# Kernel tuning notes

Measured on AMD Instinct MI355X. Metric: run time of the kernel, lower is better.

## Reference

```python
import jax, jax.numpy as jnp
import numpy as np

N_NODES = 50000
N_EDGES = 400000
FEAT = 64      # irreps_in modeled as 64 scalar channels; head_dim == FEAT
HEADS = 4


def setup_inputs() -> dict:
    key = jax.random.key(0)
    k = jax.random.split(key, 7)
    x = jax.random.normal(k[0], (N_NODES, FEAT), dtype=jnp.float32)
    edge_index = jax.random.randint(k[1], (2, N_EDGES), 0, N_NODES, dtype=jnp.int32)
    s = 1.0 / np.sqrt(FEAT)
    Wq = jax.random.normal(k[2], (HEADS, FEAT, FEAT), dtype=jnp.float32) * s
    Wk = jax.random.normal(k[3], (HEADS, FEAT, FEAT), dtype=jnp.float32) * s
    Wv = jax.random.normal(k[4], (HEADS, FEAT, FEAT), dtype=jnp.float32) * s
    Wout = jax.random.normal(k[5], (FEAT, FEAT), dtype=jnp.float32) * s
    return {"x": x, "Wq": Wq, "Wk": Wk, "Wv": Wv, "Wout": Wout, "edge_index": edge_index}


def reference(x, Wq, Wk, Wv, Wout, edge_index):
    # Per-node attention over graph neighbors. The torch module pads neighbors
    # into degree buckets and runs SDPA per bucket; mathematically this is a
    # segment (per-receiver) softmax over incoming edges, which we compute
    # directly without padding or bucket loops.
    sender, receiver = edge_index[0], edge_index[1]
    n = x.shape[0]
    scale = x.shape[1] ** -0.5  # head_dim == FEAT in the original module

    Q = jnp.einsum('nf,hfd->hnd', x, Wq)  # (H, N, F)
    K = jnp.einsum('nf,hfd->hnd', x, Wk)
    V = jnp.einsum('nf,hfd->hnd', x, Wv)

    # Edge scores: q_receiver . k_sender per head -> (E, H)
    s = jnp.einsum('hef,hef->eh', Q[:, receiver], K[:, sender]) * scale

    # Numerically stable segment softmax over each receiver's neighborhood.
    m = jax.ops.segment_max(s, receiver, num_segments=n)          # (N, H)
    p = jnp.exp(s - m[receiver])                                   # (E, H)
    denom = jax.ops.segment_sum(p, receiver, num_segments=n)      # (N, H)
    alpha = p / denom[receiver]                                    # (E, H)

    # Weighted message aggregation: (H, E, F) scattered to (H, N, F).
    msg = alpha.T[:, :, None] * V[:, sender]
    agg = jax.vmap(lambda mh: jax.ops.segment_sum(mh, receiver, num_segments=n))(msg)

    out = jnp.nan_to_num(agg.mean(axis=0))  # deg-0 nodes contribute zeros
    return x + out @ Wout
```

## Files before the change

kernel.cpp:

```cpp
#include <hip/hip_runtime.h>

#define FEAT 64
#define HEADS 4
#define CAP 64
#define LROW 520
#define TSTR 80

typedef __attribute__((ext_vector_type(8))) short short8;
typedef __attribute__((ext_vector_type(8))) __bf16 bf16x8;
typedef __attribute__((ext_vector_type(4))) float floatx4;
typedef __attribute__((ext_vector_type(2))) float float2v;
typedef unsigned short ushortT;

static __device__ __forceinline__ unsigned short f2bf(float f) {
    union { float f; unsigned int u; } v; v.f = f;
    unsigned int u = v.u;
    u = u + 0x7fffu + ((u >> 16) & 1u);
    return (unsigned short)(u >> 16);
}
static __device__ __forceinline__ float bfl(unsigned int u) {
    union { unsigned int u; float f; } v; v.u = u << 16; return v.f;
}
static __device__ __forceinline__ float bfh(unsigned int u) {
    union { unsigned int u; float f; } v; v.u = u & 0xffff0000u; return v.f;
}

__global__ __launch_bounds__(256) void k_init(const float* __restrict__ Wq,
        const float* __restrict__ Wk, const float* __restrict__ Wv,
        const float* __restrict__ Wout, short8* __restrict__ Wpack,
        short8* __restrict__ WoutPack, int4* __restrict__ deg4, int nslots) {
    int t = blockIdx.x * 256 + threadIdx.x;
    if (t < nslots) deg4[t] = make_int4(0, 0, 0, 0);
    int o = t;
    if (o < 12 * 2 * 4 * 64) {
        int lane = o & 63, dt = (o >> 6) & 3, kb = (o >> 8) & 1, m = o >> 9;
        int mat = m >> 2, h = m & 3;
        const float* src = (mat == 0) ? Wq : (mat == 1) ? Wk : Wv;
        src += (size_t)h * 64 * 64;
        int d = dt * 16 + (lane & 15);
        int kbase = kb * 32 + (lane >> 4) * 8;
        short8 val;
#pragma unroll
        for (int j = 0; j < 8; j++)
            val[j] = (short)f2bf(src[(kbase + j) * 64 + d]);
        Wpack[o] = val;
    } else if (o < 6144 + 512) {
        int idx = o - 6144;
        int lane = idx & 63, kb = (idx >> 6) & 1, nt = idx >> 7;
        int d = nt * 16 + (lane & 15);
        int kbase = kb * 32 + (lane >> 4) * 8;
        short8 val;
#pragma unroll
        for (int j = 0; j < 8; j++)
            val[j] = (short)f2bf(Wout[(kbase + j) * 64 + d]);
        WoutPack[idx] = val;
    }
}

__global__ __launch_bounds__(256) void k_qkv(const float* __restrict__ x,
        const short8* __restrict__ Wpack, const int* __restrict__ send,
        const int* __restrict__ recv, int* __restrict__ deg,
        int* __restrict__ srt, ushortT* __restrict__ Qb, ushortT* __restrict__ KVb,
        int E) {
    __shared__ ushortT lds[16 * LROW];
    int e = blockIdx.x * 256 + threadIdx.x;
    if (e < E) {
        int r = recv[e];
        int pos = atomicAdd(&deg[r], 1);
        if (pos < CAP) srt[(size_t)r * CAP + pos] = send[e];
    }

    int w = threadIdx.x >> 6, lane = threadIdx.x & 63;
    int quad = lane >> 4, lrow = lane & 15;
    int ntile = blockIdx.x * 16;
    const float* xrow = x + (size_t)(ntile + lrow) * 64 + quad * 8;
    float4 fa = *(const float4*)(xrow);
    float4 fb = *(const float4*)(xrow + 4);
    float4 fc = *(const float4*)(xrow + 32);
    float4 fd = *(const float4*)(xrow + 36);
    short8 a0 = {(short)f2bf(fa.x), (short)f2bf(fa.y), (short)f2bf(fa.z), (short)f2bf(fa.w),
                 (short)f2bf(fb.x), (short)f2bf(fb.y), (short)f2bf(fb.z), (short)f2bf(fb.w)};
    short8 a1 = {(short)f2bf(fc.x), (short)f2bf(fc.y), (short)f2bf(fc.z), (short)f2bf(fc.w),
                 (short)f2bf(fd.x), (short)f2bf(fd.y), (short)f2bf(fd.z), (short)f2bf(fd.w)};
    bf16x8 X0 = __builtin_bit_cast(bf16x8, a0);
    bf16x8 X1 = __builtin_bit_cast(bf16x8, a1);
#pragma unroll
    for (int mat = 0; mat < 3; mat++) {
        int m = mat * 4 + w;
#pragma unroll
        for (int dt = 0; dt < 4; dt++) {
            floatx4 acc = {0.f, 0.f, 0.f, 0.f};
            short8 b0 = Wpack[((m * 2 + 0) * 4 + dt) * 64 + lane];
            short8 b1 = Wpack[((m * 2 + 1) * 4 + dt) * 64 + lane];
            acc = __builtin_amdgcn_mfma_f32_16x16x32_bf16(
                __builtin_bit_cast(bf16x8, b0), X0, acc, 0, 0, 0);
            acc = __builtin_amdgcn_mfma_f32_16x16x32_bf16(
                __builtin_bit_cast(bf16x8, b1), X1, acc, 0, 0, 0);
            if (mat == 0) {
                unsigned int u01 = (unsigned)f2bf(acc[0] * 0.125f)
                                 | ((unsigned)f2bf(acc[1] * 0.125f) << 16);
                unsigned int u23 = (unsigned)f2bf(acc[2] * 0.125f)
                                 | ((unsigned)f2bf(acc[3] * 0.125f) << 16);
                *(uint2*)&lds[lrow * LROW + w * 64 + dt * 16 + quad * 4]
                    = make_uint2(u01, u23);
            } else {
                int p = __builtin_amdgcn_cvt_pk_fp8_f32(acc[0], acc[1], 0, false);
                p = __builtin_amdgcn_cvt_pk_fp8_f32(acc[2], acc[3], p, true);
                int slot = w * 16 + dt * 4 + quad;
                *(unsigned int*)&lds[lrow * LROW + 256 + slot * 4 + ((mat == 2) ? 2 : 0)]
                    = (unsigned int)p;
            }
        }
    }
    __syncthreads();
    {
        int u = threadIdx.x;
#pragma unroll
        for (int rep = 0; rep < 2; rep++, u += 256) {
            int row = u >> 5, idx = u & 31;
            uint4 val = *(const uint4*)&lds[row * LROW + idx * 8];
            *(uint4*)(Qb + ((size_t)(ntile + row)) * 256 + idx * 8) = val;
        }
    }
    {
        uint4* KVq = (uint4*)KVb;
        int u = threadIdx.x;
#pragma unroll
        for (int rep = 0; rep < 2; rep++, u += 256) {
            int row = u >> 5, idx = u & 31;
            uint4 val = *(const uint4*)&lds[row * LROW + 256 + idx * 8];
            KVq[(size_t)(ntile + row) * 32 + idx] = val;
        }
    }
}

__global__ __launch_bounds__(256) void k_attn(const ushortT* __restrict__ Qb,
        const ushortT* __restrict__ KVb, const short8* __restrict__ WoutPack,
        const int* __restrict__ deg, const int* __restrict__ srt,
        const float* __restrict__ x, float* __restrict__ out, int N) {
    __shared__ ushortT tl[16 * TSTR];
    int w = threadIdx.x >> 6, lane = threadIdx.x & 63;
    int rb = blockIdx.x * 16;
    const uint2* KV2 = (const uint2*)KVb;

    for (int rr = 0; rr < 4; rr++) {
        int ridx = w * 4 + rr;
        int r = rb + ridx;
        uint2 qu = ((const uint2*)(Qb + (size_t)r * 256))[lane];
        float q0 = bfl(qu.x), q1 = bfh(qu.x);
        float q2 = bfl(qu.y), q3 = bfh(qu.y);
        float a0 = 0.f, a1 = 0.f, a2 = 0.f, a3 = 0.f, den = 0.f;
        const int* myslots = srt + (size_t)r * CAP;
        int d = min(deg[r], CAP);

#define PROC(kv)                                                          \
    {                                                                     \
        float2v kA = __builtin_amdgcn_cvt_pk_f32_fp8(kv.x, false);        \
        float2v kB = __builtin_amdgcn_cvt_pk_f32_fp8(kv.x, true);         \
        float2v vA = __builtin_amdgcn_cvt_pk_f32_fp8(kv.y, false);        \
        float2v vB = __builtin_amdgcn_cvt_pk_f32_fp8(kv.y, true);         \
        float sp = q0 * kA.x + q1 * kA.y + q2 * kB.x + q3 * kB.y;         \
        sp += __shfl_xor(sp, 1);                                          \
        sp += __shfl_xor(sp, 2);                                          \
        sp += __shfl_xor(sp, 4);                                          \
        sp += __shfl_xor(sp, 8);                                          \
        float p = __expf(sp);                                             \
        den += p;                                                         \
        a0 += p * vA.x; a1 += p * vA.y;                                   \
        a2 += p * vB.x; a3 += p * vB.y;                                   \
    }
        int i = 0;
        for (; i + 3 < d; i += 4) {
            int4 s4 = *(const int4*)(myslots + i);
            uint2 kv0 = KV2[(size_t)s4.x * 64 + lane];
            uint2 kv1 = KV2[(size_t)s4.y * 64 + lane];
            uint2 kv2 = KV2[(size_t)s4.z * 64 + lane];
            uint2 kv3 = KV2[(size_t)s4.w * 64 + lane];
            PROC(kv0) PROC(kv1) PROC(kv2) PROC(kv3)
        }
        for (; i < d; i++) {
            uint2 kv = KV2[(size_t)myslots[i] * 64 + lane];
            PROC(kv)
        }
#undef PROC
        float inv = (den > 0.f) ? 0.25f / den : 0.f;
        a0 *= inv; a1 *= inv; a2 *= inv; a3 *= inv;
        a0 += __shfl_xor(a0, 16); a1 += __shfl_xor(a1, 16);
        a2 += __shfl_xor(a2, 16); a3 += __shfl_xor(a3, 16);
        a0 += __shfl_xor(a0, 32); a1 += __shfl_xor(a1, 32);
        a2 += __shfl_xor(a2, 32); a3 += __shfl_xor(a3, 32);
        if (lane < 16) {
            unsigned int u01 = (unsigned)f2bf(a0) | ((unsigned)f2bf(a1) << 16);
            unsigned int u23 = (unsigned)f2bf(a2) | ((unsigned)f2bf(a3) << 16);
            *(uint2*)&tl[ridx * TSTR + lane * 4] = make_uint2(u01, u23);
        }
    }
    __syncthreads();

    int q = lane >> 4, c = lane & 15;
    short8 ta0 = *(const short8*)&tl[c * TSTR + q * 8];
    short8 ta1 = *(const short8*)&tl[c * TSTR + 32 + q * 8];
    short8 tb0 = WoutPack[(w * 2 + 0) * 64 + lane];
    short8 tb1 = WoutPack[(w * 2 + 1) * 64 + lane];
    floatx4 acc = {0.f, 0.f, 0.f, 0.f};
    acc = __builtin_amdgcn_mfma_f32_16x16x32_bf16(
        __builtin_bit_cast(bf16x8, ta0), __builtin_bit_cast(bf16x8, tb0), acc, 0, 0, 0);
    acc = __builtin_amdgcn_mfma_f32_16x16x32_bf16(
        __builtin_bit_cast(bf16x8, ta1), __builtin_bit_cast(bf16x8, tb1), acc, 0, 0, 0);
#pragma unroll
    for (int reg = 0; reg < 4; reg++) {
        size_t idx = (size_t)(rb + q * 4 + reg) * 64 + w * 16 + c;
        out[idx] = x[idx] + acc[reg];
    }
}

extern "C" void kernel_launch(void* const* d_in, const int* in_sizes, int n_in,
                              void* d_out, int out_size, void* d_ws, size_t ws_size,
                              hipStream_t stream) {
    const float* x    = (const float*)d_in[0];
    const float* Wq   = (const float*)d_in[1];
    const float* Wk   = (const float*)d_in[2];
    const float* Wv   = (const float*)d_in[3];
    const float* Wout = (const float*)d_in[4];
    const int*   ei   = (const int*)d_in[5];
    int N = in_sizes[0] / FEAT;
    int E = in_sizes[5] / 2;
    const int* send = ei;
    const int* recv = ei + E;

    char* ws = (char*)d_ws;
    size_t o = 0;
    auto alloc = [&](size_t bytes) {
        void* p = ws + o;
        o = (o + bytes + 255) & ~(size_t)255;
        return p;
    };
    ushortT* Qb      = (ushortT*)alloc((size_t)N * 256 * 2);
    ushortT* KVb     = (ushortT*)alloc((size_t)N * 512);
    short8* Wpack    = (short8*)alloc(6144 * sizeof(short8));
    short8* WoutPack = (short8*)alloc(512 * sizeof(short8));
    int* deg         = (int*)alloc((size_t)((N + 3) & ~3) * 4);
    int* srt         = (int*)alloc((size_t)N * CAP * 4);

    int nslots = ((N + 3) & ~3) / 4;
    k_init<<<64, 256, 0, stream>>>(Wq, Wk, Wv, Wout, Wpack, WoutPack,
                                   (int4*)deg, nslots);
    k_qkv<<<N / 16, 256, 0, stream>>>(x, Wpack, send, recv, deg, srt, Qb, KVb, E);
    k_attn<<<N / 16, 256, 0, stream>>>(Qb, KVb, WoutPack, deg, srt, x,
                                       (float*)d_out, N);
}
```

Measured before the change: 157.3 us.

## Process two edges per wavefront with 16-byte KV loads in attention kernel

Each wavefront now splits into two half-waves that each handle a different neighbor edge. Every lane loads a uint4 with 8 K and 8 V fp8 values instead of a uint2 with 4 of each. This halves the per-edge shuffle-reduction depth and the number of loop iterations, and uses wider loads. In exchange it adds extra cross-half shuffles at the end, masked tail handling, and higher register use for the 8 accumulators.

```diff
diff --git a/kernel.cpp b/kernel.cpp
--- a/kernel.cpp
+++ b/kernel.cpp
@@ -140,59 +140,81 @@
         const float* __restrict__ x, float* __restrict__ out, int N) {
     __shared__ ushortT tl[16 * TSTR];
     int w = threadIdx.x >> 6, lane = threadIdx.x & 63;
+    int el = lane & 31, e_sel = lane >> 5, jj = lane & 7;
     int rb = blockIdx.x * 16;
-    const uint2* KV2 = (const uint2*)KVb;
+    const uint4* KV4 = (const uint4*)KVb;
 
     for (int rr = 0; rr < 4; rr++) {
         int ridx = w * 4 + rr;
         int r = rb + ridx;
-        uint2 qu = ((const uint2*)(Qb + (size_t)r * 256))[lane];
-        float q0 = bfl(qu.x), q1 = bfh(qu.x);
-        float q2 = bfl(qu.y), q3 = bfh(qu.y);
-        float a0 = 0.f, a1 = 0.f, a2 = 0.f, a3 = 0.f, den = 0.f;
+        uint4 qu = ((const uint4*)(Qb + (size_t)r * 256))[el];
+        float q0 = bfl(qu.x), q1 = bfh(qu.x), q2 = bfl(qu.y), q3 = bfh(qu.y);
+        float q4 = bfl(qu.z), q5 = bfh(qu.z), q6 = bfl(qu.w), q7 = bfh(qu.w);
+        float a0 = 0.f, a1 = 0.f, a2 = 0.f, a3 = 0.f;
+        float a4 = 0.f, a5 = 0.f, a6 = 0.f, a7 = 0.f, den = 0.f;
         const int* myslots = srt + (size_t)r * CAP;
         int d = min(deg[r], CAP);
 
-#define PROC(kv)                                                          \
+#define PROC2(kv, pmask)                                                  \
     {                                                                     \
         float2v kA = __builtin_amdgcn_cvt_pk_f32_fp8(kv.x, false);        \
         float2v kB = __builtin_amdgcn_cvt_pk_f32_fp8(kv.x, true);         \
-        float2v vA = __builtin_amdgcn_cvt_pk_f32_fp8(kv.y, false);        \
-        float2v vB = __builtin_amdgcn_cvt_pk_f32_fp8(kv.y, true);         \
-        float sp = q0 * kA.x + q1 * kA.y + q2 * kB.x + q3 * kB.y;         \
+        float2v kC = __builtin_amdgcn_cvt_pk_f32_fp8(kv.z, false);        \
+        float2v kD = __builtin_amdgcn_cvt_pk_f32_fp8(kv.z, true);         \
+        float sp = q0 * kA.x + q1 * kA.y + q2 * kB.x + q3 * kB.y          \
+                 + q4 * kC.x + q5 * kC.y + q6 * kD.x + q7 * kD.y;         \
         sp += __shfl_xor(sp, 1);                                          \
         sp += __shfl_xor(sp, 2);                                          \
         sp += __shfl_xor(sp, 4);                                          \
-        sp += __shfl_xor(sp, 8);                                          \
         float p = __expf(sp);                                             \
+        p = (pmask) ? p : 0.f;                                            \
+        float2v vA = __builtin_amdgcn_cvt_pk_f32_fp8(kv.y, false);        \
+        float2v vB = __builtin_amdgcn_cvt_pk_f32_fp8(kv.y, true);         \
+        float2v vC = __builtin_amdgcn_cvt_pk_f32_fp8(kv.w, false);        \
+        float2v vD = __builtin_amdgcn_cvt_pk_f32_fp8(kv.w, true);         \
         den += p;                                                         \
-        a0 += p * vA.x; a1 += p * vA.y;                                   \
-        a2 += p * vB.x; a3 += p * vB.y;                                   \
+        a0 += p * vA.x; a1 += p * vA.y; a2 += p * vB.x; a3 += p * vB.y;   \
+        a4 += p * vC.x; a5 += p * vC.y; a6 += p * vD.x; a7 += p * vD.y;   \
     }
         int i = 0;
         for (; i + 3 < d; i += 4) {
             int4 s4 = *(const int4*)(myslots + i);
-            uint2 kv0 = KV2[(size_t)s4.x * 64 + lane];
-            uint2 kv1 = KV2[(size_t)s4.y * 64 + lane];
-            uint2 kv2 = KV2[(size_t)s4.z * 64 + lane];
-            uint2 kv3 = KV2[(size_t)s4.w * 64 + lane];
-            PROC(kv0) PROC(kv1) PROC(kv2) PROC(kv3)
-        }
-        for (; i < d; i++) {
-            uint2 kv = KV2[(size_t)myslots[i] * 64 + lane];
-            PROC(kv)
-        }
-#undef PROC
+            int s01 = e_sel ? s4.y : s4.x;
+            int s23 = e_sel ? s4.w : s4.z;
+            uint4 kv0 = KV4[(size_t)s01 * 32 + el];
+            uint4 kv1 = KV4[(size_t)s23 * 32 + el];
+            PROC2(kv0, true) PROC2(kv1, true)
+        }
+        for (; i < d; i += 2) {
+            int idx = i + e_sel;
+            int slot = myslots[min(idx, d - 1)];
+            uint4 kv = KV4[(size_t)slot * 32 + el];
+            PROC2(kv, idx < d)
+        }
+#undef PROC2
+        den += __shfl_xor(den, 32);
+        a0 += __shfl_xor(a0, 32); a1 += __shfl_xor(a1, 32);
+        a2 += __shfl_xor(a2, 32); a3 += __shfl_xor(a3, 32);
+        a4 += __shfl_xor(a4, 32); a5 += __shfl_xor(a5, 32);
+        a6 += __shfl_xor(a6, 32); a7 += __shfl_xor(a7, 32);
         float inv = (den > 0.f) ? 0.25f / den : 0.f;
         a0 *= inv; a1 *= inv; a2 *= inv; a3 *= inv;
+        a4 *= inv; a5 *= inv; a6 *= inv; a7 *= inv;
+        a0 += __shfl_xor(a0, 8);  a1 += __shfl_xor(a1, 8);
+        a2 += __shfl_xor(a2, 8);  a3 += __shfl_xor(a3, 8);
+        a4 += __shfl_xor(a4, 8);  a5 += __shfl_xor(a5, 8);
+        a6 += __shfl_xor(a6, 8);  a7 += __shfl_xor(a7, 8);
         a0 += __shfl_xor(a0, 16); a1 += __shfl_xor(a1, 16);
         a2 += __shfl_xor(a2, 16); a3 += __shfl_xor(a3, 16);
-        a0 += __shfl_xor(a0, 32); a1 += __shfl_xor(a1, 32);
-        a2 += __shfl_xor(a2, 32); a3 += __shfl_xor(a3, 32);
-        if (lane < 16) {
-            unsigned int u01 = (unsigned)f2bf(a0) | ((unsigned)f2bf(a1) << 16);
-            unsigned int u23 = (unsigned)f2bf(a2) | ((unsigned)f2bf(a3) << 16);
-            *(uint2*)&tl[ridx * TSTR + lane * 4] = make_uint2(u01, u23);
+        a4 += __shfl_xor(a4, 16); a5 += __shfl_xor(a5, 16);
+        a6 += __shfl_xor(a6, 16); a7 += __shfl_xor(a7, 16);
+        if (lane < 8) {
+            uint4 tv;
+            tv.x = (unsigned)f2bf(a0) | ((unsigned)f2bf(a1) << 16);
+            tv.y = (unsigned)f2bf(a2) | ((unsigned)f2bf(a3) << 16);
+            tv.z = (unsigned)f2bf(a4) | ((unsigned)f2bf(a5) << 16);
+            tv.w = (unsigned)f2bf(a6) | ((unsigned)f2bf(a7) << 16);
+            *(uint4*)&tl[ridx * TSTR + jj * 8] = tv;
         }
     }
     __syncthreads();
```

New measurement: 156.9 us. About the same (-0.2%).
